# Kernel optimization log

Hardware: AMD Instinct MI355X
Metric: run time of the kernel (lower is better)

Reference implementation:

```python
import jax, jax.numpy as jnp
import numpy as np

HIDDEN = 512
ONEHOT = 64
B, L = 128, 1024


def setup_inputs() -> dict:
    key = jax.random.key(0)
    k1, k2, k3, k4, k5 = jax.random.split(key, 5)
    hidden = jax.random.normal(k1, (B, HIDDEN), dtype=jnp.float32)
    encoder_outputs = jax.random.normal(k2, (L, B, HIDDEN + ONEHOT), dtype=jnp.float32)
    # nn.Linear(2*hidden+onehot, hidden): weight (out, in), bias (out,)
    fan_in = 2 * HIDDEN + ONEHOT
    bound = 1.0 / np.sqrt(fan_in)
    W = jax.random.uniform(k3, (HIDDEN, fan_in), minval=-bound, maxval=bound, dtype=jnp.float32)
    b = jax.random.uniform(k4, (HIDDEN,), minval=-bound, maxval=bound, dtype=jnp.float32)
    stdv = 1.0 / np.sqrt(HIDDEN)
    v = jax.random.normal(k5, (HIDDEN,), dtype=jnp.float32) * stdv
    return {"hidden": hidden, "encoder_outputs": encoder_outputs, "W": W, "b": b, "v": v}


def reference(hidden, encoder_outputs, W, b, v):
    # hidden: (B, H), encoder_outputs: (L, B, H+onehot)
    h_dim = hidden.shape[1]
    enc = jnp.transpose(encoder_outputs, (1, 0, 2))  # (B, L, H+onehot)
    # Split the linear into two partial matmuls to avoid the explicit repeat+concat:
    # attn(cat([H_rep, enc])) == hidden @ Wh.T (broadcast over L) + enc @ We.T + b
    Wh = W[:, :h_dim]          # (H, H)
    We = W[:, h_dim:]          # (H, H+onehot)
    part_h = hidden @ Wh.T      # (B, H)
    part_e = jnp.einsum('bld,hd->blh', enc, We)  # (B, L, H)
    energy = jnp.tanh(part_e + part_h[:, None, :] + b)  # (B, L, H)
    scores = jnp.einsum('blh,h->bl', energy, v)          # (B, L)
    return jax.nn.softmax(scores, axis=1)[:, None, :]    # (B, 1, L)
```

## Files before the change

kernel.cpp:

```cpp
#include <hip/hip_runtime.h>
#include <stdint.h>

#define HIDDEN 512
#define ONEHOT 64
#define EDIM   576
#define BATCH  128
#define LSEQ   1024
#define FANIN  1088

typedef __attribute__((ext_vector_type(8))) short short8;
typedef __attribute__((ext_vector_type(4))) float f32x4;

__device__ inline unsigned short f2bf(float x) {
    union { float f; unsigned int u; } v; v.f = x;
    unsigned int u = v.u;
    unsigned int r = (u + 0x7FFFu + ((u >> 16) & 1u)) >> 16;
    return (unsigned short)r;
}

__device__ inline float fast_tanh(float x) {
    float ax = fabsf(x);
    float e  = __expf(2.f * ax);
    float t  = 1.f - __fdividef(2.f, e + 1.f);
    return copysignf(t, x);
}

__global__ __launch_bounds__(256) void k_prep(const float* __restrict__ hidden,
                                              const float* __restrict__ W,
                                              const float* __restrict__ bias,
                                              float* __restrict__ ph,
                                              unsigned short* __restrict__ WeB) {
    int bid = blockIdx.x;
    int tid = threadIdx.x;
    if (bid < 256) {
        int gid = bid * 256 + tid;
        int b = gid & (BATCH - 1);
        int h = gid >> 7;
        const float* hrow = hidden + b * HIDDEN;
        const float* wrow = W + h * FANIN;
        float acc = 0.f;
#pragma unroll 4
        for (int d = 0; d < HIDDEN; d += 4) {
            float4 hv = *(const float4*)(hrow + d);
            float4 wv = *(const float4*)(wrow + d);
            acc += hv.x * wv.x + hv.y * wv.y + hv.z * wv.z + hv.w * wv.w;
        }
        ph[b * HIDDEN + h] = acc + bias[h];
    } else {
        int i = (bid - 256) * 256 + tid;
        int kc = i >> 15;
        int h  = (i >> 6) & 511;
        int g  = (i >> 3) & 7;
        int j  = i & 7;
        int k  = ((g ^ (h & 7)) << 3) | j;
        WeB[i] = f2bf(W[h * FANIN + HIDDEN + kc * 64 + k]);
    }
}

#define AROW 72

__global__ __launch_bounds__(512) void k_main(
        const float* __restrict__ enc,
        const unsigned short* __restrict__ WeB,
        const float* __restrict__ ph,
        const float* __restrict__ v,
        float* __restrict__ scoresP)
{
    __shared__ unsigned short aLds[128 * AROW];
    __shared__ unsigned short bLds[128 * 64];

    const int tid  = threadIdx.x;
    const int wave = tid >> 6;
    const int lane = tid & 63;
    const int c  = lane & 15;
    const int q  = lane >> 4;
    const int vm = wave & 3;
    const int vn = wave >> 2;
    const int ht = blockIdx.x;
    const int l  = blockIdx.y;
    const int hbase = ht * 128;

    f32x4 acc[2][4];
#pragma unroll
    for (int i = 0; i < 2; ++i)
#pragma unroll
        for (int j = 0; j < 4; ++j) acc[i][j] = (f32x4){0.f, 0.f, 0.f, 0.f};

    const float* abase = enc + (size_t)l * (BATCH * EDIM);
    const char*  bsrc  = (const char*)WeB + (size_t)ht * 16384;

    for (int kc = 0; kc < 9; ++kc) {
        float4 av[4];
#pragma unroll
        for (int p = 0; p < 4; ++p) {
            int idx = p * 512 + tid;
            int row = idx >> 4;
            int c4  = idx & 15;
            av[p] = *(const float4*)(abase + row * EDIM + kc * 64 + c4 * 4);
        }

        __syncthreads();

#pragma unroll
        for (int p = 0; p < 2; ++p) {
            int off = p * 8192 + wave * 1024;
            __builtin_amdgcn_global_load_lds(
                (const __attribute__((address_space(1))) unsigned int*)
                    (bsrc + (size_t)kc * 65536 + off + lane * 16),
                (__attribute__((address_space(3))) unsigned int*)
                    ((char*)bLds + off),
                16, 0, 0);
        }

#pragma unroll
        for (int p = 0; p < 4; ++p) {
            int idx = p * 512 + tid;
            int row = idx >> 4;
            int c4  = idx & 15;
            ushort4 w;
            w.x = f2bf(av[p].x); w.y = f2bf(av[p].y);
            w.z = f2bf(av[p].z); w.w = f2bf(av[p].w);
            *(ushort4*)(&aLds[row * AROW + c4 * 4]) = w;
        }

        __syncthreads();

#pragma unroll
        for (int kk = 0; kk < 2; ++kk) {
            short8 af[2], bf[4];
#pragma unroll
            for (int am = 0; am < 2; ++am)
                af[am] = *(const short8*)(&aLds[(vm * 32 + am * 16 + c) * AROW + kk * 32 + q * 8]);
#pragma unroll
            for (int an = 0; an < 4; ++an) {
                int row = vn * 64 + an * 16 + c;
                int g   = ((kk << 2) | q) ^ (c & 7);
                bf[an]  = *(const short8*)((const char*)bLds + row * 128 + g * 16);
            }
#pragma unroll
            for (int am = 0; am < 2; ++am)
#pragma unroll
                for (int an = 0; an < 4; ++an)
                    acc[am][an] = __builtin_amdgcn_mfma_f32_16x16x32_bf16(
                        af[am], bf[an], acc[am][an], 0, 0, 0);
        }
    }

    float vv[4];
#pragma unroll
    for (int an = 0; an < 4; ++an) vv[an] = v[hbase + vn * 64 + an * 16 + c];

    const int slot = ht * 2 + vn;
#pragma unroll
    for (int am = 0; am < 2; ++am) {
#pragma unroll
        for (int r = 0; r < 4; ++r) {
            int b = vm * 32 + am * 16 + q * 4 + r;
            const float* phr = ph + b * HIDDEN + hbase + vn * 64 + c;
            float s = 0.f;
#pragma unroll
            for (int an = 0; an < 4; ++an) {
                float e = acc[am][an][r] + phr[an * 16];
                s += vv[an] * fast_tanh(e);
            }
            s += __shfl_xor(s, 1);
            s += __shfl_xor(s, 2);
            s += __shfl_xor(s, 4);
            s += __shfl_xor(s, 8);
            if (c == 0)
                scoresP[((size_t)slot * LSEQ + l) * BATCH + b] = s;
        }
    }
}

__global__ __launch_bounds__(256) void k_softmax(const float* __restrict__ sp,
                                                 float* __restrict__ out) {
    __shared__ float red[4];
    int b = blockIdx.x;
    int tid = threadIdx.x;
    float vals[4];
#pragma unroll
    for (int i = 0; i < 4; ++i) {
        int li = tid + i * 256;
        float s = 0.f;
#pragma unroll
        for (int sl = 0; sl < 8; ++sl)
            s += sp[((size_t)sl * LSEQ + li) * BATCH + b];
        vals[i] = s;
    }

    float m = fmaxf(fmaxf(vals[0], vals[1]), fmaxf(vals[2], vals[3]));
    for (int off = 1; off < 64; off <<= 1) m = fmaxf(m, __shfl_xor(m, off));
    int wv = tid >> 6;
    if ((tid & 63) == 0) red[wv] = m;
    __syncthreads();
    m = fmaxf(fmaxf(red[0], red[1]), fmaxf(red[2], red[3]));
    __syncthreads();

    float sum = 0.f;
#pragma unroll
    for (int i = 0; i < 4; ++i) { vals[i] = __expf(vals[i] - m); sum += vals[i]; }
    for (int off = 1; off < 64; off <<= 1) sum += __shfl_xor(sum, off);
    if ((tid & 63) == 0) red[wv] = sum;
    __syncthreads();
    sum = red[0] + red[1] + red[2] + red[3];
    float inv = 1.f / sum;
#pragma unroll
    for (int i = 0; i < 4; ++i)
        out[(size_t)b * LSEQ + tid + i * 256] = vals[i] * inv;
}

extern "C" void kernel_launch(void* const* d_in, const int* in_sizes, int n_in,
                              void* d_out, int out_size, void* d_ws, size_t ws_size,
                              hipStream_t stream) {
    const float* hidden = (const float*)d_in[0];
    const float* enc    = (const float*)d_in[1];
    const float* W      = (const float*)d_in[2];
    const float* bias   = (const float*)d_in[3];
    const float* v      = (const float*)d_in[4];
    float* out = (float*)d_out;

    char* ws = (char*)d_ws;
    float* ph           = (float*)ws;
    unsigned short* WeB = (unsigned short*)(ws + 262144);
    float* scoresP      = (float*)(ws + 851968);

    hipLaunchKernelGGL(k_prep, dim3(1408), dim3(256), 0, stream,
                       hidden, W, bias, ph, WeB);
    hipLaunchKernelGGL(k_main, dim3(4, 1024), dim3(512), 0, stream,
                       enc, WeB, ph, v, scoresP);
    hipLaunchKernelGGL(k_softmax, dim3(128), dim3(256), 0, stream, scoresP, out);
}
```

Measured before the change: 526.4 us.

## Widen main-kernel tile to 256 hidden columns with 1024 threads per block

```diff
diff --git a/kernel.cpp b/kernel.cpp
--- a/kernel.cpp
+++ b/kernel.cpp
@@ -59,7 +59,7 @@
 
 #define AROW 72
 
-__global__ __launch_bounds__(512) void k_main(
+__global__ __launch_bounds__(1024, 4) void k_main(
         const float* __restrict__ enc,
         const unsigned short* __restrict__ WeB,
         const float* __restrict__ ph,
@@ -67,7 +67,7 @@
         float* __restrict__ scoresP)
 {
     __shared__ unsigned short aLds[128 * AROW];
-    __shared__ unsigned short bLds[128 * 64];
+    __shared__ unsigned short bLds[256 * 64];
 
     const int tid  = threadIdx.x;
     const int wave = tid >> 6;
@@ -76,9 +76,11 @@
     const int q  = lane >> 4;
     const int vm = wave & 3;
     const int vn = wave >> 2;
-    const int ht = blockIdx.x;
-    const int l  = blockIdx.y;
-    const int hbase = ht * 128;
+
+    const int id    = blockIdx.x;
+    const int l     = (id & 7) * 128 + (id >> 4);
+    const int ht    = (id >> 3) & 1;
+    const int hbase = ht * 256;
 
     f32x4 acc[2][4];
 #pragma unroll
@@ -87,40 +89,40 @@
         for (int j = 0; j < 4; ++j) acc[i][j] = (f32x4){0.f, 0.f, 0.f, 0.f};
 
     const float* abase = enc + (size_t)l * (BATCH * EDIM);
-    const char*  bsrc  = (const char*)WeB + (size_t)ht * 16384;
+    const char*  bsrc  = (const char*)WeB + (size_t)ht * 32768;
+
+    const int row0 = tid >> 4;
+    const int c4   = tid & 15;
+    const float* ap0 = abase + (size_t)row0 * EDIM + c4 * 4;
+    const float* ap1 = ap0 + (size_t)64 * EDIM;
+    unsigned short* aw0 = &aLds[row0 * AROW + c4 * 4];
+    unsigned short* aw1 = &aLds[(row0 + 64) * AROW + c4 * 4];
 
     for (int kc = 0; kc < 9; ++kc) {
-        float4 av[4];
-#pragma unroll
-        for (int p = 0; p < 4; ++p) {
-            int idx = p * 512 + tid;
-            int row = idx >> 4;
-            int c4  = idx & 15;
-            av[p] = *(const float4*)(abase + row * EDIM + kc * 64 + c4 * 4);
-        }
+        float4 av0 = *(const float4*)(ap0 + kc * 64);
+        float4 av1 = *(const float4*)(ap1 + kc * 64);
 
         __syncthreads();
 
 #pragma unroll
         for (int p = 0; p < 2; ++p) {
-            int off = p * 8192 + wave * 1024;
+            int off = p * 16384 + wave * 1024 + lane * 16;
             __builtin_amdgcn_global_load_lds(
                 (const __attribute__((address_space(1))) unsigned int*)
-                    (bsrc + (size_t)kc * 65536 + off + lane * 16),
+                    (bsrc + (size_t)kc * 65536 + off),
                 (__attribute__((address_space(3))) unsigned int*)
                     ((char*)bLds + off),
                 16, 0, 0);
         }
 
-#pragma unroll
-        for (int p = 0; p < 4; ++p) {
-            int idx = p * 512 + tid;
-            int row = idx >> 4;
-            int c4  = idx & 15;
+        {
             ushort4 w;
-            w.x = f2bf(av[p].x); w.y = f2bf(av[p].y);
-            w.z = f2bf(av[p].z); w.w = f2bf(av[p].w);
-            *(ushort4*)(&aLds[row * AROW + c4 * 4]) = w;
+            w.x = f2bf(av0.x); w.y = f2bf(av0.y);
+            w.z = f2bf(av0.z); w.w = f2bf(av0.w);
+            *(ushort4*)aw0 = w;
+            w.x = f2bf(av1.x); w.y = f2bf(av1.y);
+            w.z = f2bf(av1.z); w.w = f2bf(av1.w);
+            *(ushort4*)aw1 = w;
         }
 
         __syncthreads();
@@ -150,7 +152,7 @@
 #pragma unroll
     for (int an = 0; an < 4; ++an) vv[an] = v[hbase + vn * 64 + an * 16 + c];
 
-    const int slot = ht * 2 + vn;
+    const int slot = ht * 4 + vn;
 #pragma unroll
     for (int am = 0; am < 2; ++am) {
 #pragma unroll
@@ -227,7 +229,7 @@
 
     hipLaunchKernelGGL(k_prep, dim3(1408), dim3(256), 0, stream,
                        hidden, W, bias, ph, WeB);
-    hipLaunchKernelGGL(k_main, dim3(4, 1024), dim3(512), 0, stream,
+    hipLaunchKernelGGL(k_main, dim3(2048), dim3(1024), 0, stream,
                        enc, WeB, ph, v, scoresP);
     hipLaunchKernelGGL(k_softmax, dim3(128), dim3(256), 0, stream, scoresP, out);
 }
```

Result: no change. 526.7 us (+0.1%).
